# Optimization experiments

Hardware: AMD Instinct MI355X
Metric: run time of the kernel (lower is better)

## Reference

```python
import jax, jax.numpy as jnp
import numpy as np

UNITS = 1024
N_CLASS = 1024
D_IN = 1024


def setup_inputs() -> dict:
    key = jax.random.key(0)
    ks = jax.random.split(key, 12)
    B, T = 128, 256
    s_in = 1.0 / np.sqrt(D_IN)
    s_h = 1.0 / np.sqrt(UNITS)
    return {
        "x": jax.random.normal(ks[0], (B, T, D_IN), jnp.float32),
        "h0": jax.random.normal(ks[1], (B, UNITS), jnp.float32),
        "c0": jax.random.normal(ks[2], (B, UNITS), jnp.float32),
        "Wk": jax.random.normal(ks[3], (D_IN, 4 * UNITS), jnp.float32) * s_in,
        "bk": jnp.zeros((4 * UNITS,), jnp.float32),
        "Wr": jax.random.normal(ks[4], (UNITS, 4 * UNITS), jnp.float32) * s_h,
        "br": jnp.zeros((4 * UNITS,), jnp.float32),
        "alpha": jax.random.normal(ks[5], (1, 4 * UNITS), jnp.float32) * 0.1,
        "beta1": jax.random.normal(ks[6], (1, 4 * UNITS), jnp.float32) * 0.1,
        "beta2": jax.random.normal(ks[7], (1, 4 * UNITS), jnp.float32) * 0.1,
        "Wc": jax.random.normal(ks[8], (UNITS, N_CLASS), jnp.float32) * s_h,
        "bc": jnp.zeros((N_CLASS,), jnp.float32),
    }


def reference(x, h0, c0, Wk, bk, Wr, br, alpha, beta1, beta2, Wc, bc):
    # x: [B, T, D_in]; scan over time (steps) with MI-LSTM cell
    def step(carry, x_t):
        h, c = carry
        xp = x_t @ Wk + bk          # [B, 4U] input projection
        hp = h @ Wr + br            # [B, 4U] recurrent projection
        z = alpha * xp * hp + beta1 * xp + beta2 * hp  # multiplicative integration
        i, f, g, o = jnp.split(z, 4, axis=1)
        c_new = jnp.tanh(g) * jax.nn.sigmoid(i) + c * jax.nn.sigmoid(f)
        h_new = jnp.tanh(c_new) * jax.nn.sigmoid(o)
        return (h_new, c_new), None

    xs = jnp.transpose(x, (1, 0, 2))  # [T, B, D_in]
    (h, c), _ = jax.lax.scan(step, (h0, c0), xs)
    out = h @ Wc + bc  # [B, n_class]
    return out, h, c
```

## Files before the change

kernel.cpp:

```cpp
#include <hip/hip_runtime.h>


typedef unsigned short u16;
typedef unsigned long long u64t;
typedef __attribute__((ext_vector_type(8))) short short8;
typedef __attribute__((ext_vector_type(4))) float f32x4;

#define B_SZ   128
#define T_SZ   256
#define D_IN   1024
#define UNITS  1024
#define FOURU  4096

__device__ __forceinline__ float bf2f(u16 h) {
    return __uint_as_float(((unsigned int)h) << 16);
}
__device__ __forceinline__ u16 f2bf(float f) {
    unsigned int u = __float_as_uint(f);
    u += 0x7fffu + ((u >> 16) & 1u);
    return (u16)(u >> 16);
}
__device__ __forceinline__ float sigmoidf_(float x) {
    return 1.0f / (1.0f + __expf(-x));
}

__global__ __launch_bounds__(256) void transpose_cvt(
    const float* __restrict__ in, u16* __restrict__ out, int K, int N)
{
    __shared__ u16 t[32][33];
    int n0 = blockIdx.x * 32, k0 = blockIdx.y * 32;
    int c = threadIdx.x & 31, r = threadIdx.x >> 5;
    #pragma unroll
    for (int i = 0; i < 4; ++i) {
        int kk = r + i * 8;
        t[kk][c] = f2bf(in[(size_t)(k0 + kk) * N + n0 + c]);
    }
    __syncthreads();
    #pragma unroll
    for (int i = 0; i < 4; ++i) {
        int nn = r + i * 8;
        out[(size_t)(n0 + nn) * K + k0 + c] = t[c][nn];
    }
}

__global__ __launch_bounds__(256) void gemm_xp_chunk(
    const float* __restrict__ X, const u16* __restrict__ Bt,
    const float* __restrict__ bias, u16* __restrict__ Cc,
    int t0, int tcShift)
{
    __shared__ __align__(16) u16 As[128 * 40];
    __shared__ __align__(16) u16 Bs[128 * 40];
    int tid = threadIdx.x;
    int wave = tid >> 6, lane = tid & 63;
    int bm = blockIdx.x * 128;
    int bn = blockIdx.y * 128;
    int wm = (wave & 1) * 64, wn = (wave >> 1) * 64;
    int lm = lane & 15, lq = lane >> 4;
    int tcMask = (1 << tcShift) - 1;

    f32x4 acc[4][4] = {};

    for (int k0 = 0; k0 < D_IN; k0 += 32) {
        #pragma unroll
        for (int i = 0; i < 2; ++i) {
            int idx = tid + i * 256;
            int r = idx >> 2, q = idx & 3;
            int rowp = bm + r;
            int b = rowp >> tcShift;
            int tt = rowp & tcMask;
            const float* xs = &X[(size_t)(b * T_SZ + t0 + tt) * D_IN + k0 + q * 8];
            float4 f0 = *(const float4*)xs;
            float4 f1 = *(const float4*)(xs + 4);
            uint4 v;
            v.x = (unsigned)f2bf(f0.x) | ((unsigned)f2bf(f0.y) << 16);
            v.y = (unsigned)f2bf(f0.z) | ((unsigned)f2bf(f0.w) << 16);
            v.z = (unsigned)f2bf(f1.x) | ((unsigned)f2bf(f1.y) << 16);
            v.w = (unsigned)f2bf(f1.z) | ((unsigned)f2bf(f1.w) << 16);
            *(uint4*)&As[r * 40 + q * 8] = v;
            *(uint4*)&Bs[r * 40 + q * 8] =
                *(const uint4*)&Bt[(size_t)(bn + r) * D_IN + k0 + q * 8];
        }
        __syncthreads();
        short8 af[4], bf[4];
        #pragma unroll
        for (int t = 0; t < 4; ++t) {
            af[t] = *(const short8*)&As[(wm + t * 16 + lm) * 40 + lq * 8];
            bf[t] = *(const short8*)&Bs[(wn + t * 16 + lm) * 40 + lq * 8];
        }
        #pragma unroll
        for (int mt = 0; mt < 4; ++mt)
            #pragma unroll
            for (int nt = 0; nt < 4; ++nt)
                acc[mt][nt] = __builtin_amdgcn_mfma_f32_16x16x32_bf16(
                    af[mt], bf[nt], acc[mt][nt], 0, 0, 0);
        __syncthreads();
    }

    #pragma unroll
    for (int mt = 0; mt < 4; ++mt) {
        #pragma unroll
        for (int nt = 0; nt < 4; ++nt) {
            int col = bn + wn + nt * 16 + lm;
            int colp = ((col & 1023) << 2) | (col >> 10);
            float bv = bias[col];
            #pragma unroll
            for (int r = 0; r < 4; ++r) {
                int rowp = bm + wm + mt * 16 + lq * 4 + r;
                Cc[(size_t)rowp * FOURU + colp] = f2bf(acc[mt][nt][r] + bv);
            }
        }
    }
}

__global__ __launch_bounds__(512) void milstm_chunk(
    const u16* __restrict__ XPc,
    const u16* __restrict__ WrT,
    const float* __restrict__ br,
    const float* __restrict__ alpha,
    const float* __restrict__ beta1,
    const float* __restrict__ beta2,
    const u16* __restrict__ h0bf,
    u16* __restrict__ hb0,
    u16* __restrict__ hb1,
    float* __restrict__ cbuf,
    unsigned* __restrict__ bar,
    int t0, int tc, int tcShift, int nbase)
{
    __shared__ __align__(16) u16 hS[16 * 1024];
    __shared__ __align__(16) float zb[2][128][20];
    __shared__ float brS[128], alS[128], b1S[128], b2S[128];

    int tid = threadIdx.x;
    int wave = tid >> 6, lane = tid & 63;
    int lm = lane & 15, lq = lane >> 4;
    int kh = wave >> 2, nq = wave & 3;
    int bid = blockIdx.x;
    int grp = bid >> 5, cb = bid & 31;
    int row0 = grp * 16;
    int ubase = cb * 32;
    unsigned gOff = (unsigned)grp * 64u;

    if (tid < 128) {
        int n = ((tid & 3) << 10) + ubase + (tid >> 2);
        brS[tid] = br[n]; alS[tid] = alpha[n];
        b1S[tid] = beta1[n]; b2S[tid] = beta2[n];
    }
    short8 Breg[32];
    #pragma unroll
    for (int j = 0; j < 16; ++j) {
        #pragma unroll
        for (int nt = 0; nt < 2; ++nt) {
            int c = nq * 32 + nt * 16 + lm;
            int n = ((c & 3) << 10) + ubase + (c >> 2);
            int k = kh * 512 + j * 32 + lq * 8;
            Breg[j * 2 + nt] = *(const short8*)&WrT[(size_t)n * 1024 + k];
        }
    }
    int erow = tid & 15, eul = tid >> 4;
    size_t hix = (size_t)(row0 + erow) * UNITS + ubase + eul;
    float cv = cbuf[hix];
    u64t xq = *(const u64t*)&XPc[((size_t)((row0 + erow) << tcShift) + 0) * FOURU
                                 + (size_t)(ubase + eul) * 4];
    int sr = tid >> 5, sc = tid & 31;
    unsigned swzS = (unsigned)((sr & 7) << 4);

    for (int s = 0; s < tc; ++s) {
        int t = t0 + s;
        const u16* hsrc = (t == 0) ? h0bf : ((t & 1) ? hb0 : hb1);
        u16* hdst = (t & 1) ? hb1 : hb0;

        {
            const u64t* hp8 = (const u64t*)&hsrc[(size_t)(row0 + sr) * UNITS] + sc * 8;
            u64t aq[8];
            #pragma unroll
            for (int i = 0; i < 8; ++i)
                aq[i] = __hip_atomic_load(hp8 + i, __ATOMIC_RELAXED, __HIP_MEMORY_SCOPE_AGENT);
            char* dst = (char*)hS + sr * 2048;
            int base = sc * 64;
            #pragma unroll
            for (int q = 0; q < 4; ++q) {
                uint4 v;
                v.x = (unsigned)aq[2 * q];     v.y = (unsigned)(aq[2 * q] >> 32);
                v.z = (unsigned)aq[2 * q + 1]; v.w = (unsigned)(aq[2 * q + 1] >> 32);
                *(uint4*)(dst + (((unsigned)(base + q * 16)) ^ swzS)) = v;
            }
        }
        __syncthreads();

        f32x4 acc0 = {}, acc1 = {};
        {
            unsigned swzA = (unsigned)((lm & 7) << 4);
            const char* hb = (const char*)hS + lm * 2048;
            #pragma unroll
            for (int j = 0; j < 16; ++j) {
                unsigned koff = (unsigned)(kh * 1024 + j * 64 + lq * 16);
                short8 a = *(const short8*)(hb + (koff ^ swzA));
                acc0 = __builtin_amdgcn_mfma_f32_16x16x32_bf16(a, Breg[j * 2],     acc0, 0, 0, 0);
                acc1 = __builtin_amdgcn_mfma_f32_16x16x32_bf16(a, Breg[j * 2 + 1], acc1, 0, 0, 0);
            }
        }
        *(f32x4*)&zb[kh][nq * 32 + lm][lq * 4]      = acc0;
        *(f32x4*)&zb[kh][nq * 32 + 16 + lm][lq * 4] = acc1;
        __syncthreads();

        {
            float zz[4];
            #pragma unroll
            for (int g = 0; g < 4; ++g) {
                int c = eul * 4 + g;
                float hp = zb[0][c][erow] + zb[1][c][erow] + brS[c];
                float xp = bf2f((u16)(xq >> (16 * g)));
                zz[g] = alS[c] * xp * hp + b1S[c] * xp + b2S[c] * hp;
            }
            float cn = tanhf(zz[2]) * sigmoidf_(zz[0]) + cv * sigmoidf_(zz[1]);
            cv = cn;
            u16 hv = f2bf(tanhf(cn) * sigmoidf_(zz[3]));
            __hip_atomic_store(&hdst[hix], hv, __ATOMIC_RELAXED, __HIP_MEMORY_SCOPE_AGENT);
        }
        if (s + 1 < tc) {
            xq = *(const u64t*)&XPc[((size_t)((row0 + erow) << tcShift) + s + 1) * FOURU
                                     + (size_t)(ubase + eul) * 4];
            __syncthreads();
            if (tid == 0) {
                unsigned barId = (unsigned)(nbase + s + 1);
                __hip_atomic_fetch_add(&bar[gOff], 1u,
                    __ATOMIC_RELAXED, __HIP_MEMORY_SCOPE_AGENT);
                while (__hip_atomic_load(&bar[gOff],
                           __ATOMIC_RELAXED, __HIP_MEMORY_SCOPE_AGENT)
                       < 32u * barId)
                    __builtin_amdgcn_s_sleep(1);
            }
            __syncthreads();
        }
    }

    cbuf[hix] = cv;
}

__global__ __launch_bounds__(256) void gemm_out(
    const u16* __restrict__ h, const u16* __restrict__ WcT,
    const float* __restrict__ bc, float* __restrict__ out)
{
    int tid = threadIdx.x;
    int wave = tid >> 6, lane = tid & 63;
    int bx = blockIdx.x;
    int row0 = (bx & 7) * 16;
    int n0 = (bx >> 3) * 64 + wave * 16;
    int lm = lane & 15, lq = lane >> 4;

    f32x4 acc = {};
    const u16* Arow = &h[(size_t)(row0 + lm) * UNITS];
    const u16* Brow = &WcT[(size_t)(n0 + lm) * UNITS];
    #pragma unroll 8
    for (int k0 = 0; k0 < UNITS; k0 += 32) {
        short8 a = *(const short8*)&Arow[k0 + lq * 8];
        short8 b = *(const short8*)&Brow[k0 + lq * 8];
        acc = __builtin_amdgcn_mfma_f32_16x16x32_bf16(a, b, acc, 0, 0, 0);
    }
    int col = n0 + lm;
    float bv = bc[col];
    #pragma unroll
    for (int r = 0; r < 4; ++r) {
        int row = row0 + lq * 4 + r;
        out[(size_t)row * 1024 + col] = acc[r] + bv;
    }
}

__global__ void cvt_f32_bf16(const float* __restrict__ in, u16* __restrict__ out, int n) {
    int i = blockIdx.x * 256 + threadIdx.x;
    if (i < n) out[i] = f2bf(in[i]);
}
__global__ void cvt_bf16_f32(const u16* __restrict__ in, float* __restrict__ out, int n) {
    int i = blockIdx.x * 256 + threadIdx.x;
    if (i < n) out[i] = bf2f(in[i]);
}
__global__ void copy_f32(const float* __restrict__ in, float* __restrict__ out, int n) {
    int i = blockIdx.x * 256 + threadIdx.x;
    if (i < n) out[i] = in[i];
}
__global__ void zero_u32(unsigned* __restrict__ p, int n) {
    int i = blockIdx.x * 256 + threadIdx.x;
    if (i < n) p[i] = 0u;
}

extern "C" void kernel_launch(void* const* d_in, const int* in_sizes, int n_in,
                              void* d_out, int out_size, void* d_ws, size_t ws_size,
                              hipStream_t stream)
{
    const float* x     = (const float*)d_in[0];
    const float* h0    = (const float*)d_in[1];
    const float* c0    = (const float*)d_in[2];
    const float* Wk    = (const float*)d_in[3];
    const float* bk    = (const float*)d_in[4];
    const float* Wr    = (const float*)d_in[5];
    const float* br    = (const float*)d_in[6];
    const float* alpha = (const float*)d_in[7];
    const float* beta1 = (const float*)d_in[8];
    const float* beta2 = (const float*)d_in[9];
    const float* Wc    = (const float*)d_in[10];
    const float* bc    = (const float*)d_in[11];
    float* out = (float*)d_out;

    char* p = (char*)d_ws;
    u16* h0bf = (u16*)p;  p += (size_t)B_SZ * UNITS * 2;
    u16* hb0  = (u16*)p;  p += (size_t)B_SZ * UNITS * 2;
    u16* hb1  = (u16*)p;  p += (size_t)B_SZ * UNITS * 2;
    float* cbuf = (float*)p; p += (size_t)B_SZ * UNITS * 4;
    unsigned* bar = (unsigned*)p; p += 8 * 64 * 4;
    u16* WkT = (u16*)p;   p += (size_t)FOURU * D_IN * 2;
    u16* WrT = (u16*)p;   p += (size_t)FOURU * UNITS * 2;
    u16* WcT = (u16*)p;   p += (size_t)1024 * 1024 * 2;
    u16* XPc = (u16*)p;

    size_t fixedB = (size_t)(p - (char*)d_ws);
    int tc = 32, tcShift = 5;
    while (tc > 1 && fixedB + (size_t)B_SZ * tc * FOURU * 2 > ws_size) {
        tc >>= 1; tcShift -= 1;
    }

    transpose_cvt<<<dim3(FOURU / 32, D_IN / 32), 256, 0, stream>>>(Wk, WkT, D_IN, FOURU);
    transpose_cvt<<<dim3(FOURU / 32, UNITS / 32), 256, 0, stream>>>(Wr, WrT, UNITS, FOURU);
    transpose_cvt<<<dim3(1024 / 32, 1024 / 32), 256, 0, stream>>>(Wc, WcT, 1024, 1024);

    cvt_f32_bf16<<<(B_SZ * UNITS) / 256, 256, 0, stream>>>(h0, h0bf, B_SZ * UNITS);
    copy_f32<<<(B_SZ * UNITS) / 256, 256, 0, stream>>>(c0, cbuf, B_SZ * UNITS);
    zero_u32<<<2, 256, 0, stream>>>(bar, 512);

    for (int t0 = 0; t0 < T_SZ; t0 += tc) {
        gemm_xp_chunk<<<dim3(tc, FOURU / 128), 256, 0, stream>>>(
            x, WkT, bk, XPc, t0, tcShift);
        int nbase = (t0 / tc) * (tc - 1);
        milstm_chunk<<<256, 512, 0, stream>>>(
            XPc, WrT, br, alpha, beta1, beta2, h0bf, hb0, hb1, cbuf, bar,
            t0, tc, tcShift, nbase);
    }

    gemm_out<<<128, 256, 0, stream>>>(hb1, WcT, bc, out);
    cvt_bf16_f32<<<(B_SZ * UNITS) / 256, 256, 0, stream>>>(hb1, out + B_SZ * UNITS, B_SZ * UNITS);
    copy_f32<<<(B_SZ * UNITS) / 256, 256, 0, stream>>>(cbuf, out + 2 * B_SZ * UNITS, B_SZ * UNITS);
}
```

Measured before the change: 2.248 ms.

## Pre-convert x to bf16, use direct global-to-LDS loads, and use hierarchical grid barrier

Adds a per-chunk kernel that converts the x slice to bf16 in workspace, so the input-projection GEMM can stage both operands with global_load_lds straight into unpadded LDS tiles instead of converting in registers. The recurrent kernel's grid barrier becomes two-level: blocks count on one of four sub-counters, and the last arrival bumps a group counter that all blocks poll. The aim is less contention on one atomic and cheaper GEMM staging. In exchange it adds an extra kernel launch and a round trip through memory for x per chunk, and the unpadded LDS layout may cause bank conflicts.

```diff
diff --git a/kernel.cpp b/kernel.cpp
--- a/kernel.cpp
+++ b/kernel.cpp
@@ -43,49 +43,65 @@
     }
 }
 
+__global__ __launch_bounds__(256) void cvt_x_chunk(
+    const float* __restrict__ x, u16* __restrict__ xb,
+    int t0, int tcShift)
+{
+    int rowp = blockIdx.x;
+    int tcMask = (1 << tcShift) - 1;
+    int b = rowp >> tcShift, tt = rowp & tcMask;
+    const float* src = &x[(size_t)(b * T_SZ + t0 + tt) * D_IN + threadIdx.x * 4];
+    float4 f = *(const float4*)src;
+    u64t v = (u64t)f2bf(f.x) | ((u64t)f2bf(f.y) << 16)
+           | ((u64t)f2bf(f.z) << 32) | ((u64t)f2bf(f.w) << 48);
+    *(u64t*)&xb[(size_t)rowp * D_IN + threadIdx.x * 4] = v;
+}
+
 __global__ __launch_bounds__(256) void gemm_xp_chunk(
-    const float* __restrict__ X, const u16* __restrict__ Bt,
-    const float* __restrict__ bias, u16* __restrict__ Cc,
-    int t0, int tcShift)
-{
-    __shared__ __align__(16) u16 As[128 * 40];
-    __shared__ __align__(16) u16 Bs[128 * 40];
+    const u16* __restrict__ xb, const u16* __restrict__ Bt,
+    const float* __restrict__ bias, u16* __restrict__ Cc)
+{
+    __shared__ __align__(16) u16 As[128 * 32];
+    __shared__ __align__(16) u16 Bs[128 * 32];
     int tid = threadIdx.x;
     int wave = tid >> 6, lane = tid & 63;
     int bm = blockIdx.x * 128;
     int bn = blockIdx.y * 128;
     int wm = (wave & 1) * 64, wn = (wave >> 1) * 64;
     int lm = lane & 15, lq = lane >> 4;
-    int tcMask = (1 << tcShift) - 1;
+
+    int r0 = (tid) >> 2,        q0 = tid & 3;
+    int r1 = (tid + 256) >> 2,  q1 = tid & 3;
 
     f32x4 acc[4][4] = {};
 
     for (int k0 = 0; k0 < D_IN; k0 += 32) {
-        #pragma unroll
-        for (int i = 0; i < 2; ++i) {
-            int idx = tid + i * 256;
-            int r = idx >> 2, q = idx & 3;
-            int rowp = bm + r;
-            int b = rowp >> tcShift;
-            int tt = rowp & tcMask;
-            const float* xs = &X[(size_t)(b * T_SZ + t0 + tt) * D_IN + k0 + q * 8];
-            float4 f0 = *(const float4*)xs;
-            float4 f1 = *(const float4*)(xs + 4);
-            uint4 v;
-            v.x = (unsigned)f2bf(f0.x) | ((unsigned)f2bf(f0.y) << 16);
-            v.y = (unsigned)f2bf(f0.z) | ((unsigned)f2bf(f0.w) << 16);
-            v.z = (unsigned)f2bf(f1.x) | ((unsigned)f2bf(f1.y) << 16);
-            v.w = (unsigned)f2bf(f1.z) | ((unsigned)f2bf(f1.w) << 16);
-            *(uint4*)&As[r * 40 + q * 8] = v;
-            *(uint4*)&Bs[r * 40 + q * 8] =
-                *(const uint4*)&Bt[(size_t)(bn + r) * D_IN + k0 + q * 8];
-        }
+        __builtin_amdgcn_global_load_lds(
+            (const __attribute__((address_space(1))) unsigned int*)
+                &xb[(size_t)(bm + r0) * D_IN + k0 + q0 * 8],
+            (__attribute__((address_space(3))) unsigned int*)&As[wave * 512],
+            16, 0, 0);
+        __builtin_amdgcn_global_load_lds(
+            (const __attribute__((address_space(1))) unsigned int*)
+                &xb[(size_t)(bm + r1) * D_IN + k0 + q1 * 8],
+            (__attribute__((address_space(3))) unsigned int*)&As[2048 + wave * 512],
+            16, 0, 0);
+        __builtin_amdgcn_global_load_lds(
+            (const __attribute__((address_space(1))) unsigned int*)
+                &Bt[(size_t)(bn + r0) * D_IN + k0 + q0 * 8],
+            (__attribute__((address_space(3))) unsigned int*)&Bs[wave * 512],
+            16, 0, 0);
+        __builtin_amdgcn_global_load_lds(
+            (const __attribute__((address_space(1))) unsigned int*)
+                &Bt[(size_t)(bn + r1) * D_IN + k0 + q1 * 8],
+            (__attribute__((address_space(3))) unsigned int*)&Bs[2048 + wave * 512],
+            16, 0, 0);
         __syncthreads();
         short8 af[4], bf[4];
         #pragma unroll
         for (int t = 0; t < 4; ++t) {
-            af[t] = *(const short8*)&As[(wm + t * 16 + lm) * 40 + lq * 8];
-            bf[t] = *(const short8*)&Bs[(wn + t * 16 + lm) * 40 + lq * 8];
+            af[t] = *(const short8*)&As[(wm + t * 16 + lm) * 32 + lq * 8];
+            bf[t] = *(const short8*)&Bs[(wn + t * 16 + lm) * 32 + lq * 8];
         }
         #pragma unroll
         for (int mt = 0; mt < 4; ++mt)
@@ -138,7 +154,8 @@
     int grp = bid >> 5, cb = bid & 31;
     int row0 = grp * 16;
     int ubase = cb * 32;
-    unsigned gOff = (unsigned)grp * 64u;
+    unsigned gOff = (unsigned)grp * 256u;
+    unsigned sub = (unsigned)(cb >> 3);
 
     if (tid < 128) {
         int n = ((tid & 3) << 10) + ubase + (tid >> 2);
@@ -223,11 +240,14 @@
             __syncthreads();
             if (tid == 0) {
                 unsigned barId = (unsigned)(nbase + s + 1);
-                __hip_atomic_fetch_add(&bar[gOff], 1u,
-                    __ATOMIC_RELAXED, __HIP_MEMORY_SCOPE_AGENT);
-                while (__hip_atomic_load(&bar[gOff],
+                unsigned old = __hip_atomic_fetch_add(&bar[gOff + sub * 32u], 1u,
+                                   __ATOMIC_RELAXED, __HIP_MEMORY_SCOPE_AGENT);
+                if (old == 8u * barId - 1u)
+                    __hip_atomic_fetch_add(&bar[gOff + 128u], 1u,
+                        __ATOMIC_RELAXED, __HIP_MEMORY_SCOPE_AGENT);
+                while (__hip_atomic_load(&bar[gOff + 128u],
                            __ATOMIC_RELAXED, __HIP_MEMORY_SCOPE_AGENT)
-                       < 32u * barId)
+                       < 4u * barId)
                     __builtin_amdgcn_s_sleep(1);
             }
             __syncthreads();
@@ -306,17 +326,18 @@
     u16* hb0  = (u16*)p;  p += (size_t)B_SZ * UNITS * 2;
     u16* hb1  = (u16*)p;  p += (size_t)B_SZ * UNITS * 2;
     float* cbuf = (float*)p; p += (size_t)B_SZ * UNITS * 4;
-    unsigned* bar = (unsigned*)p; p += 8 * 64 * 4;
+    unsigned* bar = (unsigned*)p; p += 8 * 256 * 4;
     u16* WkT = (u16*)p;   p += (size_t)FOURU * D_IN * 2;
     u16* WrT = (u16*)p;   p += (size_t)FOURU * UNITS * 2;
     u16* WcT = (u16*)p;   p += (size_t)1024 * 1024 * 2;
-    u16* XPc = (u16*)p;
 
     size_t fixedB = (size_t)(p - (char*)d_ws);
     int tc = 32, tcShift = 5;
-    while (tc > 1 && fixedB + (size_t)B_SZ * tc * FOURU * 2 > ws_size) {
+    while (tc > 1 && fixedB + (size_t)B_SZ * tc * (D_IN + FOURU * 2) > ws_size) {
         tc >>= 1; tcShift -= 1;
     }
+    u16* xb  = (u16*)p;   p += (size_t)B_SZ * tc * D_IN * 2;
+    u16* XPc = (u16*)p;
 
     transpose_cvt<<<dim3(FOURU / 32, D_IN / 32), 256, 0, stream>>>(Wk, WkT, D_IN, FOURU);
     transpose_cvt<<<dim3(FOURU / 32, UNITS / 32), 256, 0, stream>>>(Wr, WrT, UNITS, FOURU);
@@ -324,11 +345,12 @@
 
     cvt_f32_bf16<<<(B_SZ * UNITS) / 256, 256, 0, stream>>>(h0, h0bf, B_SZ * UNITS);
     copy_f32<<<(B_SZ * UNITS) / 256, 256, 0, stream>>>(c0, cbuf, B_SZ * UNITS);
-    zero_u32<<<2, 256, 0, stream>>>(bar, 512);
+    zero_u32<<<8, 256, 0, stream>>>(bar, 2048);
 
     for (int t0 = 0; t0 < T_SZ; t0 += tc) {
+        cvt_x_chunk<<<B_SZ * tc, 256, 0, stream>>>(x, xb, t0, tcShift);
         gemm_xp_chunk<<<dim3(tc, FOURU / 128), 256, 0, stream>>>(
-            x, WkT, bk, XPc, t0, tcShift);
+            xb, WkT, bk, XPc);
         int nbase = (t0 / tc) * (tc - 1);
         milstm_chunk<<<256, 512, 0, stream>>>(
             XPc, WrT, br, alpha, beta1, beta2, h0bf, hb0, hb1, cbuf, bar,
```

After: 2.146 ms. 1.05x faster.
